# Kernel optimization log

Measured on AMD Instinct MI355X. Metric: run time of the kernel, lower is better.

The kernel has to match this reference:

```python
import jax, jax.numpy as jnp
import numpy as np

N_ATOMS, N_UND, N_DIR, N_ANG, N_STRUCT = 8192, 65536, 131072, 262144, 128
FEA, NRAD, NANGB, NCONV = 64, 9, 9, 4

FLOAT_NAMES = ["bond_bases_ag", "bond_bases_bg", "angle_bases", "atom_emb", "Wb", "Wa",
               "Wbw_ag", "Wbw_bg",
               "ac_cw1", "ac_cb1", "ac_cw2", "ac_cb2", "ac_gw1", "ac_gb1", "ac_gw2", "ac_gb2", "ac_out",
               "bc_cw1", "bc_cb1", "bc_cw2", "bc_cb2", "bc_gw1", "bc_gb1", "bc_gw2", "bc_gb2", "bc_out",
               "an_cw", "an_cb", "an_gw", "an_gb",
               "ro_w1", "ro_b1", "ro_w2", "ro_b2", "ro_w3", "ro_b3"]
INT_NAMES = ["atomic_numbers", "atom_graph", "directed2undirected",
             "bond_graph_atoms", "bond_graph_bonds", "atom_owners"]


def _silu(x):
    return x * jax.nn.sigmoid(x)


def _gmlp(x, cw1, cb1, cw2, cb2, gw1, gb1, gw2, gb2):
    # GatedMLP (norm=None): silu(MLP_core(x)) * sigmoid(MLP_gate(x)), each MLP = Lin-silu-Lin
    core = _silu(_silu(x @ cw1 + cb1) @ cw2 + cb2)
    gate = jax.nn.sigmoid(_silu(x @ gw1 + gb1) @ gw2 + gb2)
    return core * gate


def _forward(F, I):
    seg = jax.ops.segment_sum
    atom = F["atom_emb"][I["atomic_numbers"]]            # [N, 64]
    bond = F["bond_bases_ag"] @ F["Wb"]                  # [U, 64]
    angle = F["angle_bases"] @ F["Wa"]                   # [A, 64]
    bw_ag = F["bond_bases_ag"] @ F["Wbw_ag"]             # [U, 64]
    bw_bg = F["bond_bases_bg"] @ F["Wbw_bg"]             # [U, 64]
    ag0, ag1 = I["atom_graph"][:, 0], I["atom_graph"][:, 1]
    d2u = I["directed2undirected"]
    bgi, bgj = I["bond_graph_bonds"][:, 0], I["bond_graph_bonds"][:, 1]
    bga = I["bond_graph_atoms"]

    def atom_conv(i, atom, bond):
        msg = jnp.concatenate([atom[ag0], bond[d2u], atom[ag1]], axis=1)   # [E, 192]
        msg = _gmlp(msg, F["ac_cw1"][i], F["ac_cb1"][i], F["ac_cw2"][i], F["ac_cb2"][i],
                    F["ac_gw1"][i], F["ac_gb1"][i], F["ac_gw2"][i], F["ac_gb2"][i])
        msg = msg * bw_ag[d2u]
        # scatter-add to center atoms, linear mlp_out (no bias), resnet
        return atom + seg(msg, ag0, num_segments=N_ATOMS) @ F["ac_out"][i]

    for i in range(NCONV - 1):
        atom = atom_conv(i, atom, bond)
        # BondConv over bond graph (angles)
        tot = jnp.concatenate([bond[bgi], bond[bgj], angle, atom[bga]], axis=1)  # [A, 256]
        upd = _gmlp(tot, F["bc_cw1"][i], F["bc_cb1"][i], F["bc_cw2"][i], F["bc_cb2"][i],
                    F["bc_gw1"][i], F["bc_gb1"][i], F["bc_gw2"][i], F["bc_gb2"][i])
        upd = upd * bw_bg[bgi]
        bond = bond + seg(upd, bgi, num_segments=N_UND) @ F["bc_out"][i]
        # AngleUpdate (hidden_dim=0 -> single linear in each gated branch), resnet
        tot2 = jnp.concatenate([bond[bgi], bond[bgj], angle, atom[bga]], axis=1)
        angle = angle + _silu(tot2 @ F["an_cw"][i] + F["an_cb"][i]) * \
            jax.nn.sigmoid(tot2 @ F["an_gw"][i] + F["an_gb"][i])
    atom = atom_conv(NCONV - 1, atom, bond)

    # mlp_first readout: per-atom energy MLP then average pooling per structure
    e = _silu(atom @ F["ro_w1"] + F["ro_b1"])
    e = _silu(e @ F["ro_w2"] + F["ro_b2"])
    e = (e @ F["ro_w3"] + F["ro_b3"])[:, 0]              # [N]
    owners = I["atom_owners"]
    esum = seg(e, owners, num_segments=N_STRUCT)
    cnt = seg(jnp.ones_like(e), owners, num_segments=N_STRUCT)
    return esum / jnp.maximum(cnt, 1.0)                  # [N_STRUCT] energy/atom


def setup_inputs() -> dict:
    key = jax.random.key(0)
    ks = iter(jax.random.split(key, 64))

    def nrm(shape, fan_in):
        return jax.random.normal(next(ks), shape, dtype=jnp.float32) / np.float32(np.sqrt(fan_in))

    z = lambda *s: jnp.zeros(s, dtype=jnp.float32)
    inp = {}
    inp["atomic_numbers"] = jax.random.randint(next(ks), (N_ATOMS,), 0, 94, dtype=jnp.int32)
    inp["bond_bases_ag"] = jax.random.uniform(next(ks), (N_UND, NRAD), dtype=jnp.float32)
    inp["bond_bases_bg"] = jax.random.uniform(next(ks), (N_UND, NRAD), dtype=jnp.float32)
    inp["angle_bases"] = jax.random.uniform(next(ks), (N_ANG, NANGB), dtype=jnp.float32)
    inp["atom_graph"] = jax.random.randint(next(ks), (N_DIR, 2), 0, N_ATOMS, dtype=jnp.int32)
    inp["directed2undirected"] = jax.random.randint(next(ks), (N_DIR,), 0, N_UND, dtype=jnp.int32)
    inp["bond_graph_atoms"] = jax.random.randint(next(ks), (N_ANG,), 0, N_ATOMS, dtype=jnp.int32)
    inp["bond_graph_bonds"] = jax.random.randint(next(ks), (N_ANG, 2), 0, N_UND, dtype=jnp.int32)
    inp["atom_owners"] = jnp.sort(jax.random.randint(next(ks), (N_ATOMS,), 0, N_STRUCT, dtype=jnp.int32))
    inp["atom_emb"] = nrm((95, FEA), 1.0)
    inp["Wb"] = nrm((NRAD, FEA), NRAD)
    inp["Wa"] = nrm((NANGB, FEA), NANGB)
    inp["Wbw_ag"] = nrm((NRAD, FEA), NRAD)
    inp["Wbw_bg"] = nrm((NRAD, FEA), NRAD)
    d_a, d_b = 3 * FEA, 4 * FEA
    nb = NCONV - 1
    inp["ac_cw1"] = nrm((NCONV, d_a, FEA), d_a); inp["ac_cb1"] = z(NCONV, FEA)
    inp["ac_cw2"] = nrm((NCONV, FEA, FEA), FEA); inp["ac_cb2"] = z(NCONV, FEA)
    inp["ac_gw1"] = nrm((NCONV, d_a, FEA), d_a); inp["ac_gb1"] = z(NCONV, FEA)
    inp["ac_gw2"] = nrm((NCONV, FEA, FEA), FEA); inp["ac_gb2"] = z(NCONV, FEA)
    inp["ac_out"] = nrm((NCONV, FEA, FEA), FEA)
    inp["bc_cw1"] = nrm((nb, d_b, FEA), d_b); inp["bc_cb1"] = z(nb, FEA)
    inp["bc_cw2"] = nrm((nb, FEA, FEA), FEA); inp["bc_cb2"] = z(nb, FEA)
    inp["bc_gw1"] = nrm((nb, d_b, FEA), d_b); inp["bc_gb1"] = z(nb, FEA)
    inp["bc_gw2"] = nrm((nb, FEA, FEA), FEA); inp["bc_gb2"] = z(nb, FEA)
    inp["bc_out"] = nrm((nb, FEA, FEA), FEA)
    inp["an_cw"] = nrm((nb, d_b, FEA), d_b); inp["an_cb"] = z(nb, FEA)
    inp["an_gw"] = nrm((nb, d_b, FEA), d_b); inp["an_gb"] = z(nb, FEA)
    inp["ro_w1"] = nrm((FEA, FEA), FEA); inp["ro_b1"] = z(FEA)
    inp["ro_w2"] = nrm((FEA, FEA), FEA); inp["ro_b2"] = z(FEA)
    inp["ro_w3"] = nrm((FEA, 1), FEA); inp["ro_b3"] = z(1)
    return inp


def reference(atomic_numbers, bond_bases_ag, bond_bases_bg, angle_bases, atom_graph,
              directed2undirected, bond_graph_atoms, bond_graph_bonds, atom_owners,
              atom_emb, Wb, Wa, Wbw_ag, Wbw_bg,
              ac_cw1, ac_cb1, ac_cw2, ac_cb2, ac_gw1, ac_gb1, ac_gw2, ac_gb2, ac_out,
              bc_cw1, bc_cb1, bc_cw2, bc_cb2, bc_gw1, bc_gb1, bc_gw2, bc_gb2, bc_out,
              an_cw, an_cb, an_gw, an_gb,
              ro_w1, ro_b1, ro_w2, ro_b2, ro_w3, ro_b3):
    loc = locals()
    F = {k: loc[k] for k in FLOAT_NAMES}
    I = {k: loc[k] for k in INT_NAMES}
    return _forward(F, I)
```

## Files before the change

kernel.cpp:

```cpp
#include <hip/hip_runtime.h>
#include <hip/hip_bf16.h>

typedef float f32x4 __attribute__((ext_vector_type(4)));
typedef short s16x8 __attribute__((ext_vector_type(8)));
typedef unsigned int u32x4 __attribute__((ext_vector_type(4)));

#define DEV static __device__ __forceinline__

DEV unsigned short f2bf(float x){
    unsigned u = __builtin_bit_cast(unsigned, x);
    u += 0x7FFFu + ((u >> 16) & 1u);
    return (unsigned short)(u >> 16);
}
DEV float bf2f(unsigned short h){
    unsigned u = ((unsigned)h) << 16;
    return __builtin_bit_cast(float, u);
}
DEV float sigm_(float x){ return __builtin_amdgcn_rcpf(1.0f + __expf(-x)); }
DEV float silu_(float x){ return x * sigm_(x); }

DEV int xcd_swz(){
    int bid = blockIdx.x, nwg = gridDim.x;
    return (bid & 7) * (nwg >> 3) + (bid >> 3);
}

__global__ __launch_bounds__(256) void k_transconv(const float* __restrict__ src,
                                                   unsigned short* __restrict__ dst,
                                                   int K, int total){
    int gid = blockIdx.x * 256 + threadIdx.x;
    if (gid >= total) return;
    int kn  = K * 64;
    int b   = gid / kn;
    int rem = gid - b * kn;
    int k   = rem >> 6, n = rem & 63;
    dst[b * kn + n * K + k] = f2bf(src[gid]);
}

__global__ __launch_bounds__(256) void k_embed(const float* __restrict__ emb,
                                               const int* __restrict__ z,
                                               unsigned short* __restrict__ out){
    int gid = blockIdx.x * 256 + threadIdx.x;
    int n = gid >> 6, f = gid & 63;
    out[gid] = f2bf(emb[z[n] * 64 + f]);
}

__global__ __launch_bounds__(256) void k_smallmm(const float* __restrict__ bases,
                                                 const float* __restrict__ W,
                                                 unsigned short* __restrict__ out){
    int gid = blockIdx.x * 256 + threadIdx.x;
    int r = gid >> 6, f = gid & 63;
    const float* b = bases + r * 9;
    float acc = 0.f;
    #pragma unroll
    for (int k = 0; k < 9; ++k) acc += b[k] * W[k * 64 + f];
    out[gid] = f2bf(acc);
}

__global__ void k_count(const int* __restrict__ dst, int stride, int n, int* __restrict__ cnt){
    int i = blockIdx.x * 256 + threadIdx.x;
    if (i < n) atomicAdd(&cnt[dst[(size_t)i * stride]], 1);
}

__global__ __launch_bounds__(256) void k_bsum(const int* __restrict__ cnt,
                                              int* __restrict__ bsum){
    int i = blockIdx.x * 256 + threadIdx.x;
    int v = cnt[i];
    #pragma unroll
    for (int off = 32; off > 0; off >>= 1) v += __shfl_down(v, off);
    __shared__ int ws[4];
    if ((threadIdx.x & 63) == 0) ws[threadIdx.x >> 6] = v;
    __syncthreads();
    if (threadIdx.x == 0) bsum[blockIdx.x] = ws[0] + ws[1] + ws[2] + ws[3];
}

__global__ __launch_bounds__(256) void k_bscan(const int* __restrict__ bsum,
                                               int* __restrict__ bbase, int nb,
                                               int* __restrict__ total_out){
    __shared__ int sh[256];
    int t = threadIdx.x;
    int v = (t < nb) ? bsum[t] : 0;
    sh[t] = v;
    __syncthreads();
    for (int d = 1; d < 256; d <<= 1){
        int u = (t >= d) ? sh[t - d] : 0;
        __syncthreads();
        sh[t] += u;
        __syncthreads();
    }
    if (t < nb) bbase[t] = sh[t] - v;
    if (t == nb - 1) *total_out = sh[t];
}

__global__ __launch_bounds__(256) void k_offs(const int* __restrict__ cnt,
                                              const int* __restrict__ bbase,
                                              int* __restrict__ offs){
    __shared__ int sh[256];
    int t = threadIdx.x;
    int i = blockIdx.x * 256 + t;
    int v = cnt[i];
    sh[t] = v;
    __syncthreads();
    for (int d = 1; d < 256; d <<= 1){
        int u = (t >= d) ? sh[t - d] : 0;
        __syncthreads();
        sh[t] += u;
        __syncthreads();
    }
    offs[i] = bbase[blockIdx.x] + sh[t] - v;
}

__global__ void k_fill(const int* __restrict__ dst, int stride, int n,
                       const int* __restrict__ offs, int* __restrict__ cur,
                       int* __restrict__ idx){
    int i = blockIdx.x * 256 + threadIdx.x;
    if (i < n){
        int d = dst[(size_t)i * stride];
        int p = offs[d] + atomicAdd(&cur[d], 1);
        idx[p] = i;
    }
}

__global__ __launch_bounds__(256) void k_reduce(const unsigned short* __restrict__ upd,
                                                const int* __restrict__ offs,
                                                unsigned short* __restrict__ act, int nRows){
    int gid = blockIdx.x * 256 + threadIdx.x;
    int row = gid >> 3;
    if (row >= nRows) return;
    int c8 = (gid & 7) * 8;
    int o = offs[row], e = offs[row + 1];
    float acc[8] = {};
    for (int j = o; j < e; ++j){
        s16x8 v = *(const s16x8*)&upd[(size_t)j * 64 + c8];
        #pragma unroll
        for (int q = 0; q < 8; ++q) acc[q] += bf2f((unsigned short)v[q]);
    }
    s16x8 a = *(s16x8*)&act[(size_t)row * 64 + c8];
    #pragma unroll
    for (int q = 0; q < 8; ++q) a[q] = (short)f2bf(bf2f((unsigned short)a[q]) + acc[q]);
    *(s16x8*)&act[(size_t)row * 64 + c8] = a;
}

#define MFMA16(a,b,c) __builtin_amdgcn_mfma_f32_16x16x32_bf16(a,b,c,0,0,0)

__global__ __launch_bounds__(256, 4) void k_atom_conv(
    const unsigned short* __restrict__ atomBf, const unsigned short* __restrict__ bondBf,
    const unsigned short* __restrict__ bwagBf,
    const int* __restrict__ agraph, const int* __restrict__ d2u,
    const int* __restrict__ idxA,
    const unsigned short* __restrict__ w1cT, const unsigned short* __restrict__ w1gT,
    const unsigned short* __restrict__ w2cT, const unsigned short* __restrict__ w2gT,
    const unsigned short* __restrict__ woT,
    const float* __restrict__ cb1, const float* __restrict__ cb2,
    const float* __restrict__ gb1, const float* __restrict__ gb2,
    unsigned short* __restrict__ upd)
{
    __shared__ unsigned short lds[14208];
    __shared__ unsigned short ldsBw[64 * 68];
    __shared__ int ldsSrc[256];
    unsigned short* ldsA  = lds;
    unsigned short* ldsHC = lds;
    unsigned short* ldsHG = lds + 4736;
    unsigned short* ldsV  = lds + 9472;
    const int tid = threadIdx.x;
    const int r0  = xcd_swz() * 64;

    {
        int q = tid >> 6, row = tid & 63;
        int e = idxA[r0 + row];
        int s;
        if (q == 0)      s = agraph[2 * e];
        else if (q == 1) s = d2u[e];
        else if (q == 2) s = agraph[2 * e + 1];
        else             s = d2u[e];
        ldsSrc[tid] = s;
    }
    __syncthreads();
    {
        const int lane8 = tid & 7;
        #pragma unroll
        for (int p = 0; p < 8; ++p){
            int cc = p * 32 + (tid >> 3);
            int q = cc >> 6, row = cc & 63;
            int s = ldsSrc[cc];
            const unsigned short* buf = (q == 1 || q == 3) ? bondBf : atomBf;
            if (q == 3) buf = bwagBf;
            u32x4 v = *(const u32x4*)(buf + (size_t)s * 64 + lane8 * 8);
            if (q < 3) *(u32x4*)&ldsA[row * 200 + q * 64 + lane8 * 8] = v;
            else       *(u32x4*)&ldsBw[row * 68 + lane8 * 8] = v;
        }
    }
    __syncthreads();

    const int lane = tid & 63;
    const int r16  = lane & 15;
    const int grp  = lane >> 4;
    const int col  = (tid >> 6) * 16 + r16;

    f32x4 aC[4] = {}, aG[4] = {};
    #pragma unroll
    for (int kt = 0; kt < 6; ++kt){
        s16x8 bc = *(const s16x8*)&w1cT[col * 192 + kt * 32 + grp * 8];
        s16x8 bg = *(const s16x8*)&w1gT[col * 192 + kt * 32 + grp * 8];
        #pragma unroll
        for (int mt = 0; mt < 4; ++mt){
            s16x8 a = *(const s16x8*)&ldsA[(mt * 16 + r16) * 200 + kt * 32 + grp * 8];
            aC[mt] = MFMA16(a, bc, aC[mt]);
            aG[mt] = MFMA16(a, bg, aG[mt]);
        }
    }
    __syncthreads();

    const float bC1 = cb1[col], bG1 = gb1[col];
    #pragma unroll
    for (int mt = 0; mt < 4; ++mt){
        #pragma unroll
        for (int j = 0; j < 4; ++j){
            int row = mt * 16 + grp * 4 + j;
            ldsHC[row * 74 + col] = f2bf(silu_(aC[mt][j] + bC1));
            ldsHG[row * 74 + col] = f2bf(silu_(aG[mt][j] + bG1));
        }
    }
    __syncthreads();

    f32x4 oC[4] = {}, oG[4] = {};
    #pragma unroll
    for (int kt = 0; kt < 2; ++kt){
        s16x8 bc = *(const s16x8*)&w2cT[col * 64 + kt * 32 + grp * 8];
        s16x8 bg = *(const s16x8*)&w2gT[col * 64 + kt * 32 + grp * 8];
        #pragma unroll
        for (int mt = 0; mt < 4; ++mt){
            s16x8 hc = *(const s16x8*)&ldsHC[(mt * 16 + r16) * 74 + kt * 32 + grp * 8];
            s16x8 hg = *(const s16x8*)&ldsHG[(mt * 16 + r16) * 74 + kt * 32 + grp * 8];
            oC[mt] = MFMA16(hc, bc, oC[mt]);
            oG[mt] = MFMA16(hg, bg, oG[mt]);
        }
    }
    const float bC2 = cb2[col], bG2 = gb2[col];
    #pragma unroll
    for (int mt = 0; mt < 4; ++mt){
        #pragma unroll
        for (int j = 0; j < 4; ++j){
            int row = mt * 16 + grp * 4 + j;
            float v = silu_(oC[mt][j] + bC2) * sigm_(oG[mt][j] + bG2);
            v *= bf2f(ldsBw[row * 68 + col]);
            ldsV[row * 74 + col] = f2bf(v);
        }
    }
    __syncthreads();

    f32x4 oD[4] = {};
    #pragma unroll
    for (int kt = 0; kt < 2; ++kt){
        s16x8 bo = *(const s16x8*)&woT[col * 64 + kt * 32 + grp * 8];
        #pragma unroll
        for (int mt = 0; mt < 4; ++mt){
            s16x8 a = *(const s16x8*)&ldsV[(mt * 16 + r16) * 74 + kt * 32 + grp * 8];
            oD[mt] = MFMA16(a, bo, oD[mt]);
        }
    }
    #pragma unroll
    for (int mt = 0; mt < 4; ++mt){
        #pragma unroll
        for (int j = 0; j < 4; ++j){
            int row = mt * 16 + grp * 4 + j;
            upd[(size_t)(r0 + row) * 64 + col] = f2bf(oD[mt][j]);
        }
    }
}

__global__ __launch_bounds__(256, 4) void k_bond_conv(
    const unsigned short* __restrict__ atomBf, const unsigned short* __restrict__ bondBf,
    const unsigned short* __restrict__ angleBf, const unsigned short* __restrict__ bwbgBf,
    const int* __restrict__ bga, const int* __restrict__ bgb,
    const int* __restrict__ idxB,
    const unsigned short* __restrict__ w1cT, const unsigned short* __restrict__ w1gT,
    const unsigned short* __restrict__ w2cT, const unsigned short* __restrict__ w2gT,
    const unsigned short* __restrict__ woT,
    const float* __restrict__ cb1, const float* __restrict__ cb2,
    const float* __restrict__ gb1, const float* __restrict__ gb2,
    unsigned short* __restrict__ upd)
{
    __shared__ unsigned short lds[16896];
    __shared__ int ldsSrc[256];
    unsigned short* ldsA  = lds;
    unsigned short* ldsHC = lds;
    unsigned short* ldsHG = lds + 4736;
    unsigned short* ldsV  = lds + 9472;
    const int tid = threadIdx.x;
    const int r0  = xcd_swz() * 64;

    {
        int q = tid >> 6, row = tid & 63;
        int a = idxB[r0 + row];
        int s;
        if (q == 0)      s = bgb[2 * a];
        else if (q == 1) s = bgb[2 * a + 1];
        else if (q == 2) s = a;
        else             s = bga[a];
        ldsSrc[tid] = s;
    }
    __syncthreads();
    {
        const int lane8 = tid & 7;
        #pragma unroll
        for (int p = 0; p < 8; ++p){
            int cc = p * 32 + (tid >> 3);
            int q = cc >> 6, row = cc & 63;
            int s = ldsSrc[cc];
            const unsigned short* buf = (q < 2) ? bondBf : (q == 2 ? angleBf : atomBf);
            u32x4 v = *(const u32x4*)(buf + (size_t)s * 64 + lane8 * 8);
            *(u32x4*)&ldsA[row * 264 + q * 64 + lane8 * 8] = v;
        }
    }
    __syncthreads();

    const int lane = tid & 63;
    const int r16  = lane & 15;
    const int grp  = lane >> 4;
    const int col  = (tid >> 6) * 16 + r16;

    unsigned short bwv[16];
    #pragma unroll
    for (int mt = 0; mt < 4; ++mt)
        #pragma unroll
        for (int j = 0; j < 4; ++j)
            bwv[mt * 4 + j] = bwbgBf[(size_t)ldsSrc[mt * 16 + grp * 4 + j] * 64 + col];

    f32x4 aC[4] = {}, aG[4] = {};
    #pragma unroll
    for (int kt = 0; kt < 8; ++kt){
        s16x8 bc = *(const s16x8*)&w1cT[col * 256 + kt * 32 + grp * 8];
        s16x8 bg = *(const s16x8*)&w1gT[col * 256 + kt * 32 + grp * 8];
        #pragma unroll
        for (int mt = 0; mt < 4; ++mt){
            s16x8 a = *(const s16x8*)&ldsA[(mt * 16 + r16) * 264 + kt * 32 + grp * 8];
            aC[mt] = MFMA16(a, bc, aC[mt]);
            aG[mt] = MFMA16(a, bg, aG[mt]);
        }
    }
    __syncthreads();

    const float bC1 = cb1[col], bG1 = gb1[col];
    #pragma unroll
    for (int mt = 0; mt < 4; ++mt){
        #pragma unroll
        for (int j = 0; j < 4; ++j){
            int row = mt * 16 + grp * 4 + j;
            ldsHC[row * 74 + col] = f2bf(silu_(aC[mt][j] + bC1));
            ldsHG[row * 74 + col] = f2bf(silu_(aG[mt][j] + bG1));
        }
    }
    __syncthreads();

    f32x4 oC[4] = {}, oG[4] = {};
    #pragma unroll
    for (int kt = 0; kt < 2; ++kt){
        s16x8 bc = *(const s16x8*)&w2cT[col * 64 + kt * 32 + grp * 8];
        s16x8 bg = *(const s16x8*)&w2gT[col * 64 + kt * 32 + grp * 8];
        #pragma unroll
        for (int mt = 0; mt < 4; ++mt){
            s16x8 hc = *(const s16x8*)&ldsHC[(mt * 16 + r16) * 74 + kt * 32 + grp * 8];
            s16x8 hg = *(const s16x8*)&ldsHG[(mt * 16 + r16) * 74 + kt * 32 + grp * 8];
            oC[mt] = MFMA16(hc, bc, oC[mt]);
            oG[mt] = MFMA16(hg, bg, oG[mt]);
        }
    }
    const float bC2 = cb2[col], bG2 = gb2[col];
    #pragma unroll
    for (int mt = 0; mt < 4; ++mt){
        #pragma unroll
        for (int j = 0; j < 4; ++j){
            int row = mt * 16 + grp * 4 + j;
            float v = silu_(oC[mt][j] + bC2) * sigm_(oG[mt][j] + bG2);
            v *= bf2f(bwv[mt * 4 + j]);
            ldsV[row * 74 + col] = f2bf(v);
        }
    }
    __syncthreads();

    f32x4 oD[4] = {};
    #pragma unroll
    for (int kt = 0; kt < 2; ++kt){
        s16x8 bo = *(const s16x8*)&woT[col * 64 + kt * 32 + grp * 8];
        #pragma unroll
        for (int mt = 0; mt < 4; ++mt){
            s16x8 a = *(const s16x8*)&ldsV[(mt * 16 + r16) * 74 + kt * 32 + grp * 8];
            oD[mt] = MFMA16(a, bo, oD[mt]);
        }
    }
    #pragma unroll
    for (int mt = 0; mt < 4; ++mt){
        #pragma unroll
        for (int j = 0; j < 4; ++j){
            int row = mt * 16 + grp * 4 + j;
            upd[(size_t)(r0 + row) * 64 + col] = f2bf(oD[mt][j]);
        }
    }
}

__global__ __launch_bounds__(256, 4) void k_angle(
    const unsigned short* __restrict__ atomBf, const unsigned short* __restrict__ bondBf,
    unsigned short* __restrict__ angleBf,
    const int* __restrict__ bga, const int* __restrict__ bgb,
    const int* __restrict__ idxB,
    const unsigned short* __restrict__ wcT, const unsigned short* __restrict__ wgT,
    const float* __restrict__ cb, const float* __restrict__ gb)
{
    __shared__ unsigned short ldsA[64 * 264];
    __shared__ int ldsSrc[256];
    const int tid = threadIdx.x;
    const int r0  = xcd_swz() * 64;

    {
        int q = tid >> 6, row = tid & 63;
        int a = idxB[r0 + row];
        int s;
        if (q == 0)      s = bgb[2 * a];
        else if (q == 1) s = bgb[2 * a + 1];
        else if (q == 2) s = a;
        else             s = bga[a];
        ldsSrc[tid] = s;
    }
    __syncthreads();
    {
        const int lane8 = tid & 7;
        #pragma unroll
        for (int p = 0; p < 8; ++p){
            int cc = p * 32 + (tid >> 3);
            int q = cc >> 6, row = cc & 63;
            int s = ldsSrc[cc];
            const unsigned short* buf = (q < 2) ? bondBf : (q == 2 ? angleBf : atomBf);
            u32x4 v = *(const u32x4*)(buf + (size_t)s * 64 + lane8 * 8);
            *(u32x4*)&ldsA[row * 264 + q * 64 + lane8 * 8] = v;
        }
    }
    __syncthreads();

    const int lane = tid & 63;
    const int r16  = lane & 15;
    const int grp  = lane >> 4;
    const int col  = (tid >> 6) * 16 + r16;

    f32x4 aC[4] = {}, aG[4] = {};
    #pragma unroll
    for (int kt = 0; kt < 8; ++kt){
        s16x8 bc = *(const s16x8*)&wcT[col * 256 + kt * 32 + grp * 8];
        s16x8 bg = *(const s16x8*)&wgT[col * 256 + kt * 32 + grp * 8];
        #pragma unroll
        for (int mt = 0; mt < 4; ++mt){
            s16x8 a = *(const s16x8*)&ldsA[(mt * 16 + r16) * 264 + kt * 32 + grp * 8];
            aC[mt] = MFMA16(a, bc, aC[mt]);
            aG[mt] = MFMA16(a, bg, aG[mt]);
        }
    }
    const float bC = cb[col], bG = gb[col];
    #pragma unroll
    for (int mt = 0; mt < 4; ++mt){
        #pragma unroll
        for (int j = 0; j < 4; ++j){
            int row = mt * 16 + grp * 4 + j;
            int a = ldsSrc[128 + row];
            float oldv = bf2f(ldsA[row * 264 + 128 + col]);
            float v = silu_(aC[mt][j] + bC) * sigm_(aG[mt][j] + bG);
            angleBf[(size_t)a * 64 + col] = f2bf(oldv + v);
        }
    }
}

__global__ __launch_bounds__(256) void k_readout(
    const unsigned short* __restrict__ atomBf, const int* __restrict__ owners,
    const float* __restrict__ w1, const float* __restrict__ b1,
    const float* __restrict__ w2, const float* __restrict__ b2,
    const float* __restrict__ w3, const float* __restrict__ b3,
    float* __restrict__ esum, float* __restrict__ cnt)
{
    int gid  = blockIdx.x * 256 + threadIdx.x;
    int n    = gid >> 6;
    int lane = threadIdx.x & 63;
    float a = bf2f(atomBf[n * 64 + lane]);
    float acc = b1[lane];
    #pragma unroll
    for (int k = 0; k < 64; ++k) acc += __shfl(a, k) * w1[k * 64 + lane];
    float h = silu_(acc);
    acc = b2[lane];
    #pragma unroll
    for (int k = 0; k < 64; ++k) acc += __shfl(h, k) * w2[k * 64 + lane];
    h = silu_(acc);
    float p = h * w3[lane];
    #pragma unroll
    for (int off = 32; off > 0; off >>= 1) p += __shfl_xor(p, off);
    if (lane == 0){
        atomicAdd(&esum[owners[n]], p + b3[0]);
        atomicAdd(&cnt[owners[n]], 1.0f);
    }
}

__global__ void k_final(const float* __restrict__ esum, const float* __restrict__ cnt,
                        float* __restrict__ out){
    int i = threadIdx.x;
    if (i < 128) out[i] = esum[i] / fmaxf(cnt[i], 1.0f);
}

extern "C" void kernel_launch(void* const* d_in, const int* in_sizes, int n_in,
                              void* d_out, int out_size, void* d_ws, size_t ws_size,
                              hipStream_t stream)
{
    (void)in_sizes; (void)n_in; (void)out_size; (void)ws_size;
    const int N_ATOMS = 8192, N_UND = 65536, N_DIR = 131072, N_ANG = 262144;

    const int*   atomic_numbers = (const int*)  d_in[0];
    const float* bb_ag  = (const float*)d_in[1];
    const float* bb_bg  = (const float*)d_in[2];
    const float* ang_b  = (const float*)d_in[3];
    const int*   agraph = (const int*)  d_in[4];
    const int*   d2u    = (const int*)  d_in[5];
    const int*   bga    = (const int*)  d_in[6];
    const int*   bgb    = (const int*)  d_in[7];
    const int*   owners = (const int*)  d_in[8];
    const float* emb    = (const float*)d_in[9];
    const float* Wb     = (const float*)d_in[10];
    const float* Wa     = (const float*)d_in[11];
    const float* Wbwag  = (const float*)d_in[12];
    const float* Wbwbg  = (const float*)d_in[13];
    const float* ac_cw1 = (const float*)d_in[14];
    const float* ac_cb1 = (const float*)d_in[15];
    const float* ac_cw2 = (const float*)d_in[16];
    const float* ac_cb2 = (const float*)d_in[17];
    const float* ac_gw1 = (const float*)d_in[18];
    const float* ac_gb1 = (const float*)d_in[19];
    const float* ac_gw2 = (const float*)d_in[20];
    const float* ac_gb2 = (const float*)d_in[21];
    const float* ac_out = (const float*)d_in[22];
    const float* bc_cw1 = (const float*)d_in[23];
    const float* bc_cb1 = (const float*)d_in[24];
    const float* bc_cw2 = (const float*)d_in[25];
    const float* bc_cb2 = (const float*)d_in[26];
    const float* bc_gw1 = (const float*)d_in[27];
    const float* bc_gb1 = (const float*)d_in[28];
    const float* bc_gw2 = (const float*)d_in[29];
    const float* bc_gb2 = (const float*)d_in[30];
    const float* bc_out = (const float*)d_in[31];
    const float* an_cw  = (const float*)d_in[32];
    const float* an_cb  = (const float*)d_in[33];
    const float* an_gw  = (const float*)d_in[34];
    const float* an_gb  = (const float*)d_in[35];
    const float* ro_w1  = (const float*)d_in[36];
    const float* ro_b1  = (const float*)d_in[37];
    const float* ro_w2  = (const float*)d_in[38];
    const float* ro_b2  = (const float*)d_in[39];
    const float* ro_w3  = (const float*)d_in[40];
    const float* ro_b3  = (const float*)d_in[41];

    char* ws = (char*)d_ws;
    size_t off = 0;
    auto alloc = [&](size_t bytes) -> void* {
        void* p = ws + off;
        off = (off + bytes + 255) & ~(size_t)255;
        return p;
    };
    unsigned short* atomBf  = (unsigned short*)alloc((size_t)N_ATOMS * 64 * 2);
    unsigned short* bondBf  = (unsigned short*)alloc((size_t)N_UND   * 64 * 2);
    unsigned short* angleBf = (unsigned short*)alloc((size_t)N_ANG   * 64 * 2);
    unsigned short* bwagBf  = (unsigned short*)alloc((size_t)N_UND   * 64 * 2);
    unsigned short* bwbgBf  = (unsigned short*)alloc((size_t)N_UND   * 64 * 2);
    unsigned short* updBuf  = (unsigned short*)alloc((size_t)N_ANG   * 64 * 2);
    float* esum   = (float*)alloc(128 * 4);
    float* cnt    = (float*)alloc(128 * 4);
    int* offsA = (int*)alloc((N_ATOMS + 1) * 4);
    int* curA  = (int*)alloc(N_ATOMS * 4);
    int* idxA  = (int*)alloc((size_t)N_DIR * 4);
    int* offsB = (int*)alloc((N_UND + 1) * 4);
    int* curB  = (int*)alloc(N_UND * 4);
    int* idxB  = (int*)alloc((size_t)N_ANG * 4);
    int* bsum  = (int*)alloc(256 * 4);
    int* bbase = (int*)alloc(256 * 4);
    unsigned short* acw1cT = (unsigned short*)alloc((size_t)4 * 64 * 192 * 2);
    unsigned short* acw1gT = (unsigned short*)alloc((size_t)4 * 64 * 192 * 2);
    unsigned short* acw2cT = (unsigned short*)alloc((size_t)4 * 64 * 64 * 2);
    unsigned short* acw2gT = (unsigned short*)alloc((size_t)4 * 64 * 64 * 2);
    unsigned short* acoT   = (unsigned short*)alloc((size_t)4 * 64 * 64 * 2);
    unsigned short* bcw1cT = (unsigned short*)alloc((size_t)3 * 64 * 256 * 2);
    unsigned short* bcw1gT = (unsigned short*)alloc((size_t)3 * 64 * 256 * 2);
    unsigned short* bcw2cT = (unsigned short*)alloc((size_t)3 * 64 * 64 * 2);
    unsigned short* bcw2gT = (unsigned short*)alloc((size_t)3 * 64 * 64 * 2);
    unsigned short* bcoT   = (unsigned short*)alloc((size_t)3 * 64 * 64 * 2);
    unsigned short* anwcT  = (unsigned short*)alloc((size_t)3 * 64 * 256 * 2);
    unsigned short* anwgT  = (unsigned short*)alloc((size_t)3 * 64 * 256 * 2);

    auto tc = [&](const float* src, unsigned short* dst, int B, int K){
        int total = B * K * 64;
        k_transconv<<<(total + 255) / 256, 256, 0, stream>>>(src, dst, K, total);
    };
    tc(ac_cw1, acw1cT, 4, 192);  tc(ac_gw1, acw1gT, 4, 192);
    tc(ac_cw2, acw2cT, 4, 64);   tc(ac_gw2, acw2gT, 4, 64);
    tc(ac_out, acoT,   4, 64);
    tc(bc_cw1, bcw1cT, 3, 256);  tc(bc_gw1, bcw1gT, 3, 256);
    tc(bc_cw2, bcw2cT, 3, 64);   tc(bc_gw2, bcw2gT, 3, 64);
    tc(bc_out, bcoT,   3, 64);
    tc(an_cw,  anwcT,  3, 256);  tc(an_gw,  anwgT,  3, 256);

    k_embed<<<N_ATOMS * 64 / 256, 256, 0, stream>>>(emb, atomic_numbers, atomBf);
    k_smallmm<<<N_UND * 64 / 256, 256, 0, stream>>>(bb_ag, Wb,    bondBf);
    k_smallmm<<<N_ANG * 64 / 256, 256, 0, stream>>>(ang_b, Wa,    angleBf);
    k_smallmm<<<N_UND * 64 / 256, 256, 0, stream>>>(bb_ag, Wbwag, bwagBf);
    k_smallmm<<<N_UND * 64 / 256, 256, 0, stream>>>(bb_bg, Wbwbg, bwbgBf);

    hipMemsetAsync(curA, 0, N_ATOMS * 4, stream);
    k_count<<<(N_DIR + 255) / 256, 256, 0, stream>>>(agraph, 2, N_DIR, curA);
    k_bsum <<<N_ATOMS / 256, 256, 0, stream>>>(curA, bsum);
    k_bscan<<<1, 256, 0, stream>>>(bsum, bbase, N_ATOMS / 256, offsA + N_ATOMS);
    k_offs <<<N_ATOMS / 256, 256, 0, stream>>>(curA, bbase, offsA);
    hipMemsetAsync(curA, 0, N_ATOMS * 4, stream);
    k_fill<<<(N_DIR + 255) / 256, 256, 0, stream>>>(agraph, 2, N_DIR, offsA, curA, idxA);

    hipMemsetAsync(curB, 0, N_UND * 4, stream);
    k_count<<<(N_ANG + 255) / 256, 256, 0, stream>>>(bgb, 2, N_ANG, curB);
    k_bsum <<<N_UND / 256, 256, 0, stream>>>(curB, bsum);
    k_bscan<<<1, 256, 0, stream>>>(bsum, bbase, N_UND / 256, offsB + N_UND);
    k_offs <<<N_UND / 256, 256, 0, stream>>>(curB, bbase, offsB);
    hipMemsetAsync(curB, 0, N_UND * 4, stream);
    k_fill<<<(N_ANG + 255) / 256, 256, 0, stream>>>(bgb, 2, N_ANG, offsB, curB, idxB);

    for (int i = 0; i < 4; ++i){
        k_atom_conv<<<N_DIR / 64, 256, 0, stream>>>(
            atomBf, bondBf, bwagBf, agraph, d2u, idxA,
            acw1cT + (size_t)i * 64 * 192, acw1gT + (size_t)i * 64 * 192,
            acw2cT + (size_t)i * 64 * 64,  acw2gT + (size_t)i * 64 * 64,
            acoT   + (size_t)i * 64 * 64,
            ac_cb1 + i * 64, ac_cb2 + i * 64, ac_gb1 + i * 64, ac_gb2 + i * 64, updBuf);
        k_reduce<<<N_ATOMS * 8 / 256, 256, 0, stream>>>(updBuf, offsA, atomBf, N_ATOMS);
        if (i == 3) break;
        k_bond_conv<<<N_ANG / 64, 256, 0, stream>>>(
            atomBf, bondBf, angleBf, bwbgBf, bga, bgb, idxB,
            bcw1cT + (size_t)i * 64 * 256, bcw1gT + (size_t)i * 64 * 256,
            bcw2cT + (size_t)i * 64 * 64,  bcw2gT + (size_t)i * 64 * 64,
            bcoT   + (size_t)i * 64 * 64,
            bc_cb1 + i * 64, bc_cb2 + i * 64, bc_gb1 + i * 64, bc_gb2 + i * 64, updBuf);
        k_reduce<<<N_UND * 8 / 256, 256, 0, stream>>>(updBuf, offsB, bondBf, N_UND);
        k_angle<<<N_ANG / 64, 256, 0, stream>>>(
            atomBf, bondBf, angleBf, bga, bgb, idxB,
            anwcT + (size_t)i * 64 * 256, anwgT + (size_t)i * 64 * 256,
            an_cb + i * 64, an_gb + i * 64);
    }

    hipMemsetAsync(esum, 0, 128 * 4, stream);
    hipMemsetAsync(cnt,  0, 128 * 4, stream);
    k_readout<<<N_ATOMS * 64 / 256, 256, 0, stream>>>(
        atomBf, owners, ro_w1, ro_b1, ro_w2, ro_b2, ro_w3, ro_b3, esum, cnt);
    k_final<<<1, 128, 0, stream>>>(esum, cnt, (float*)d_out);
}
```

Baseline: 870.9 us.

## Store angles in bond-sorted order and fuse angle update with next atom conv

Angle features are now built directly in the idxB-sorted order, so the bond conv and angle kernels read them with contiguous indices instead of gathering, and the angle update writes back without a scatter. The angle update and the following atom conv, which are independent, run as one combined launch with the block range split between the two bodies. This saves launches and fills the GPU better, at the cost of shared-memory sizing set by the larger body and the loss of XCD swizzling in the fused kernel. The fused atom path writes updBuf while angle blocks only touch angleS, so there is no conflict.

```diff
diff --git a/kernel.cpp b/kernel.cpp
--- a/kernel.cpp
+++ b/kernel.cpp
@@ -50,6 +50,19 @@
     int gid = blockIdx.x * 256 + threadIdx.x;
     int r = gid >> 6, f = gid & 63;
     const float* b = bases + r * 9;
+    float acc = 0.f;
+    #pragma unroll
+    for (int k = 0; k < 9; ++k) acc += b[k] * W[k * 64 + f];
+    out[gid] = f2bf(acc);
+}
+
+__global__ __launch_bounds__(256) void k_smallmm_perm(const float* __restrict__ bases,
+                                                      const float* __restrict__ W,
+                                                      const int* __restrict__ perm,
+                                                      unsigned short* __restrict__ out){
+    int gid = blockIdx.x * 256 + threadIdx.x;
+    int r = gid >> 6, f = gid & 63;
+    const float* b = bases + (size_t)perm[r] * 9;
     float acc = 0.f;
     #pragma unroll
     for (int k = 0; k < 9; ++k) acc += b[k] * W[k * 64 + f];
@@ -141,6 +154,195 @@
 }
 
 #define MFMA16(a,b,c) __builtin_amdgcn_mfma_f32_16x16x32_bf16(a,b,c,0,0,0)
+
+DEV void atom_body(unsigned short* smem, int* ldsSrc, int bid,
+    const unsigned short* atomBf, const unsigned short* bondBf,
+    const unsigned short* bwagBf,
+    const int* agraph, const int* d2u, const int* idxA,
+    const unsigned short* w1cT, const unsigned short* w1gT,
+    const unsigned short* w2cT, const unsigned short* w2gT,
+    const unsigned short* woT,
+    const float* cb1, const float* cb2, const float* gb1, const float* gb2,
+    unsigned short* upd)
+{
+    unsigned short* ldsA  = smem;
+    unsigned short* ldsHC = smem;
+    unsigned short* ldsHG = smem + 4736;
+    unsigned short* ldsV  = smem + 9472;
+    unsigned short* ldsBw = smem + 14208;
+    const int tid = threadIdx.x;
+    const int r0  = bid * 64;
+
+    {
+        int q = tid >> 6, row = tid & 63;
+        int e = idxA[r0 + row];
+        int s;
+        if (q == 0)      s = agraph[2 * e];
+        else if (q == 1) s = d2u[e];
+        else if (q == 2) s = agraph[2 * e + 1];
+        else             s = d2u[e];
+        ldsSrc[tid] = s;
+    }
+    __syncthreads();
+    {
+        const int lane8 = tid & 7;
+        #pragma unroll
+        for (int p = 0; p < 8; ++p){
+            int cc = p * 32 + (tid >> 3);
+            int q = cc >> 6, row = cc & 63;
+            int s = ldsSrc[cc];
+            const unsigned short* buf = (q == 1 || q == 3) ? bondBf : atomBf;
+            if (q == 3) buf = bwagBf;
+            u32x4 v = *(const u32x4*)(buf + (size_t)s * 64 + lane8 * 8);
+            if (q < 3) *(u32x4*)&ldsA[row * 200 + q * 64 + lane8 * 8] = v;
+            else       *(u32x4*)&ldsBw[row * 68 + lane8 * 8] = v;
+        }
+    }
+    __syncthreads();
+
+    const int lane = tid & 63;
+    const int r16  = lane & 15;
+    const int grp  = lane >> 4;
+    const int col  = (tid >> 6) * 16 + r16;
+
+    f32x4 aC[4] = {}, aG[4] = {};
+    #pragma unroll
+    for (int kt = 0; kt < 6; ++kt){
+        s16x8 bc = *(const s16x8*)&w1cT[col * 192 + kt * 32 + grp * 8];
+        s16x8 bg = *(const s16x8*)&w1gT[col * 192 + kt * 32 + grp * 8];
+        #pragma unroll
+        for (int mt = 0; mt < 4; ++mt){
+            s16x8 a = *(const s16x8*)&ldsA[(mt * 16 + r16) * 200 + kt * 32 + grp * 8];
+            aC[mt] = MFMA16(a, bc, aC[mt]);
+            aG[mt] = MFMA16(a, bg, aG[mt]);
+        }
+    }
+    __syncthreads();
+
+    const float bC1 = cb1[col], bG1 = gb1[col];
+    #pragma unroll
+    for (int mt = 0; mt < 4; ++mt){
+        #pragma unroll
+        for (int j = 0; j < 4; ++j){
+            int row = mt * 16 + grp * 4 + j;
+            ldsHC[row * 74 + col] = f2bf(silu_(aC[mt][j] + bC1));
+            ldsHG[row * 74 + col] = f2bf(silu_(aG[mt][j] + bG1));
+        }
+    }
+    __syncthreads();
+
+    f32x4 oC[4] = {}, oG[4] = {};
+    #pragma unroll
+    for (int kt = 0; kt < 2; ++kt){
+        s16x8 bc = *(const s16x8*)&w2cT[col * 64 + kt * 32 + grp * 8];
+        s16x8 bg = *(const s16x8*)&w2gT[col * 64 + kt * 32 + grp * 8];
+        #pragma unroll
+        for (int mt = 0; mt < 4; ++mt){
+            s16x8 hc = *(const s16x8*)&ldsHC[(mt * 16 + r16) * 74 + kt * 32 + grp * 8];
+            s16x8 hg = *(const s16x8*)&ldsHG[(mt * 16 + r16) * 74 + kt * 32 + grp * 8];
+            oC[mt] = MFMA16(hc, bc, oC[mt]);
+            oG[mt] = MFMA16(hg, bg, oG[mt]);
+        }
+    }
+    const float bC2 = cb2[col], bG2 = gb2[col];
+    #pragma unroll
+    for (int mt = 0; mt < 4; ++mt){
+        #pragma unroll
+        for (int j = 0; j < 4; ++j){
+            int row = mt * 16 + grp * 4 + j;
+            float v = silu_(oC[mt][j] + bC2) * sigm_(oG[mt][j] + bG2);
+            v *= bf2f(ldsBw[row * 68 + col]);
+            ldsV[row * 74 + col] = f2bf(v);
+        }
+    }
+    __syncthreads();
+
+    f32x4 oD[4] = {};
+    #pragma unroll
+    for (int kt = 0; kt < 2; ++kt){
+        s16x8 bo = *(const s16x8*)&woT[col * 64 + kt * 32 + grp * 8];
+        #pragma unroll
+        for (int mt = 0; mt < 4; ++mt){
+            s16x8 a = *(const s16x8*)&ldsV[(mt * 16 + r16) * 74 + kt * 32 + grp * 8];
+            oD[mt] = MFMA16(a, bo, oD[mt]);
+        }
+    }
+    #pragma unroll
+    for (int mt = 0; mt < 4; ++mt){
+        #pragma unroll
+        for (int j = 0; j < 4; ++j){
+            int row = mt * 16 + grp * 4 + j;
+            upd[(size_t)(r0 + row) * 64 + col] = f2bf(oD[mt][j]);
+        }
+    }
+}
+
+DEV void angle_body(unsigned short* ldsA, int* ldsSrc, int bid,
+    const unsigned short* atomBf, const unsigned short* bondBf,
+    unsigned short* angleS,
+    const int* bga, const int* bgb, const int* idxB,
+    const unsigned short* wcT, const unsigned short* wgT,
+    const float* cb, const float* gb)
+{
+    const int tid = threadIdx.x;
+    const int r0  = bid * 64;
+
+    {
+        int q = tid >> 6, row = tid & 63;
+        int s;
+        if (q == 2) s = r0 + row;
+        else {
+            int a = idxB[r0 + row];
+            if (q == 0)      s = bgb[2 * a];
+            else if (q == 1) s = bgb[2 * a + 1];
+            else             s = bga[a];
+        }
+        ldsSrc[tid] = s;
+    }
+    __syncthreads();
+    {
+        const int lane8 = tid & 7;
+        #pragma unroll
+        for (int p = 0; p < 8; ++p){
+            int cc = p * 32 + (tid >> 3);
+            int q = cc >> 6, row = cc & 63;
+            int s = ldsSrc[cc];
+            const unsigned short* buf = (q < 2) ? bondBf : (q == 2 ? angleS : atomBf);
+            u32x4 v = *(const u32x4*)(buf + (size_t)s * 64 + lane8 * 8);
+            *(u32x4*)&ldsA[row * 264 + q * 64 + lane8 * 8] = v;
+        }
+    }
+    __syncthreads();
+
+    const int lane = tid & 63;
+    const int r16  = lane & 15;
+    const int grp  = lane >> 4;
+    const int col  = (tid >> 6) * 16 + r16;
+
+    f32x4 aC[4] = {}, aG[4] = {};
+    #pragma unroll
+    for (int kt = 0; kt < 8; ++kt){
+        s16x8 bc = *(const s16x8*)&wcT[col * 256 + kt * 32 + grp * 8];
+        s16x8 bg = *(const s16x8*)&wgT[col * 256 + kt * 32 + grp * 8];
+        #pragma unroll
+        for (int mt = 0; mt < 4; ++mt){
+            s16x8 a = *(const s16x8*)&ldsA[(mt * 16 + r16) * 264 + kt * 32 + grp * 8];
+            aC[mt] = MFMA16(a, bc, aC[mt]);
+            aG[mt] = MFMA16(a, bg, aG[mt]);
+        }
+    }
+    const float bC = cb[col], bG = gb[col];
+    #pragma unroll
+    for (int mt = 0; mt < 4; ++mt){
+        #pragma unroll
+        for (int j = 0; j < 4; ++j){
+            int row = mt * 16 + grp * 4 + j;
+            float oldv = bf2f(ldsA[row * 264 + 128 + col]);
+            float v = silu_(aC[mt][j] + bC) * sigm_(aG[mt][j] + bG);
+            angleS[(size_t)(r0 + row) * 64 + col] = f2bf(oldv + v);
+        }
+    }
+}
 
 __global__ __launch_bounds__(256, 4) void k_atom_conv(
     const unsigned short* __restrict__ atomBf, const unsigned short* __restrict__ bondBf,
@@ -154,123 +356,44 @@
     const float* __restrict__ gb1, const float* __restrict__ gb2,
     unsigned short* __restrict__ upd)
 {
-    __shared__ unsigned short lds[14208];
-    __shared__ unsigned short ldsBw[64 * 68];
+    __shared__ __align__(16) unsigned short smem[18560];
     __shared__ int ldsSrc[256];
-    unsigned short* ldsA  = lds;
-    unsigned short* ldsHC = lds;
-    unsigned short* ldsHG = lds + 4736;
-    unsigned short* ldsV  = lds + 9472;
-    const int tid = threadIdx.x;
-    const int r0  = xcd_swz() * 64;
-
-    {
-        int q = tid >> 6, row = tid & 63;
-        int e = idxA[r0 + row];
-        int s;
-        if (q == 0)      s = agraph[2 * e];
-        else if (q == 1) s = d2u[e];
-        else if (q == 2) s = agraph[2 * e + 1];
-        else             s = d2u[e];
-        ldsSrc[tid] = s;
-    }
-    __syncthreads();
-    {
-        const int lane8 = tid & 7;
-        #pragma unroll
-        for (int p = 0; p < 8; ++p){
-            int cc = p * 32 + (tid >> 3);
-            int q = cc >> 6, row = cc & 63;
-            int s = ldsSrc[cc];
-            const unsigned short* buf = (q == 1 || q == 3) ? bondBf : atomBf;
-            if (q == 3) buf = bwagBf;
-            u32x4 v = *(const u32x4*)(buf + (size_t)s * 64 + lane8 * 8);
-            if (q < 3) *(u32x4*)&ldsA[row * 200 + q * 64 + lane8 * 8] = v;
-            else       *(u32x4*)&ldsBw[row * 68 + lane8 * 8] = v;
-        }
-    }
-    __syncthreads();
-
-    const int lane = tid & 63;
-    const int r16  = lane & 15;
-    const int grp  = lane >> 4;
-    const int col  = (tid >> 6) * 16 + r16;
-
-    f32x4 aC[4] = {}, aG[4] = {};
-    #pragma unroll
-    for (int kt = 0; kt < 6; ++kt){
-        s16x8 bc = *(const s16x8*)&w1cT[col * 192 + kt * 32 + grp * 8];
-        s16x8 bg = *(const s16x8*)&w1gT[col * 192 + kt * 32 + grp * 8];
-        #pragma unroll
-        for (int mt = 0; mt < 4; ++mt){
-            s16x8 a = *(const s16x8*)&ldsA[(mt * 16 + r16) * 200 + kt * 32 + grp * 8];
-            aC[mt] = MFMA16(a, bc, aC[mt]);
-            aG[mt] = MFMA16(a, bg, aG[mt]);
-        }
-    }
-    __syncthreads();
-
-    const float bC1 = cb1[col], bG1 = gb1[col];
-    #pragma unroll
-    for (int mt = 0; mt < 4; ++mt){
-        #pragma unroll
-        for (int j = 0; j < 4; ++j){
-            int row = mt * 16 + grp * 4 + j;
-            ldsHC[row * 74 + col] = f2bf(silu_(aC[mt][j] + bC1));
-            ldsHG[row * 74 + col] = f2bf(silu_(aG[mt][j] + bG1));
-        }
-    }
-    __syncthreads();
-
-    f32x4 oC[4] = {}, oG[4] = {};
-    #pragma unroll
-    for (int kt = 0; kt < 2; ++kt){
-        s16x8 bc = *(const s16x8*)&w2cT[col * 64 + kt * 32 + grp * 8];
-        s16x8 bg = *(const s16x8*)&w2gT[col * 64 + kt * 32 + grp * 8];
-        #pragma unroll
-        for (int mt = 0; mt < 4; ++mt){
-            s16x8 hc = *(const s16x8*)&ldsHC[(mt * 16 + r16) * 74 + kt * 32 + grp * 8];
-            s16x8 hg = *(const s16x8*)&ldsHG[(mt * 16 + r16) * 74 + kt * 32 + grp * 8];
-            oC[mt] = MFMA16(hc, bc, oC[mt]);
-            oG[mt] = MFMA16(hg, bg, oG[mt]);
-        }
-    }
-    const float bC2 = cb2[col], bG2 = gb2[col];
-    #pragma unroll
-    for (int mt = 0; mt < 4; ++mt){
-        #pragma unroll
-        for (int j = 0; j < 4; ++j){
-            int row = mt * 16 + grp * 4 + j;
-            float v = silu_(oC[mt][j] + bC2) * sigm_(oG[mt][j] + bG2);
-            v *= bf2f(ldsBw[row * 68 + col]);
-            ldsV[row * 74 + col] = f2bf(v);
-        }
-    }
-    __syncthreads();
-
-    f32x4 oD[4] = {};
-    #pragma unroll
-    for (int kt = 0; kt < 2; ++kt){
-        s16x8 bo = *(const s16x8*)&woT[col * 64 + kt * 32 + grp * 8];
-        #pragma unroll
-        for (int mt = 0; mt < 4; ++mt){
-            s16x8 a = *(const s16x8*)&ldsV[(mt * 16 + r16) * 74 + kt * 32 + grp * 8];
-            oD[mt] = MFMA16(a, bo, oD[mt]);
-        }
-    }
-    #pragma unroll
-    for (int mt = 0; mt < 4; ++mt){
-        #pragma unroll
-        for (int j = 0; j < 4; ++j){
-            int row = mt * 16 + grp * 4 + j;
-            upd[(size_t)(r0 + row) * 64 + col] = f2bf(oD[mt][j]);
-        }
+    atom_body(smem, ldsSrc, xcd_swz(),
+              atomBf, bondBf, bwagBf, agraph, d2u, idxA,
+              w1cT, w1gT, w2cT, w2gT, woT, cb1, cb2, gb1, gb2, upd);
+}
+
+__global__ __launch_bounds__(256, 4) void k_angle_atom(
+    const unsigned short* __restrict__ atomBf, const unsigned short* __restrict__ bondBf,
+    unsigned short* __restrict__ angleS, const unsigned short* __restrict__ bwagBf,
+    const int* __restrict__ agraph, const int* __restrict__ d2u, const int* __restrict__ idxA,
+    const int* __restrict__ bga, const int* __restrict__ bgb, const int* __restrict__ idxB,
+    const unsigned short* __restrict__ an_wcT, const unsigned short* __restrict__ an_wgT,
+    const float* __restrict__ an_cb, const float* __restrict__ an_gb,
+    const unsigned short* __restrict__ ac_w1cT, const unsigned short* __restrict__ ac_w1gT,
+    const unsigned short* __restrict__ ac_w2cT, const unsigned short* __restrict__ ac_w2gT,
+    const unsigned short* __restrict__ ac_woT,
+    const float* __restrict__ ac_cb1, const float* __restrict__ ac_cb2,
+    const float* __restrict__ ac_gb1, const float* __restrict__ ac_gb2,
+    unsigned short* __restrict__ upd, int nbAngle)
+{
+    __shared__ __align__(16) unsigned short smem[18560];
+    __shared__ int ldsSrc[256];
+    int bid = blockIdx.x;
+    if (bid < nbAngle){
+        angle_body(smem, ldsSrc, bid, atomBf, bondBf, angleS, bga, bgb, idxB,
+                   an_wcT, an_wgT, an_cb, an_gb);
+    } else {
+        atom_body(smem, ldsSrc, bid - nbAngle,
+                  atomBf, bondBf, bwagBf, agraph, d2u, idxA,
+                  ac_w1cT, ac_w1gT, ac_w2cT, ac_w2gT, ac_woT,
+                  ac_cb1, ac_cb2, ac_gb1, ac_gb2, upd);
     }
 }
 
 __global__ __launch_bounds__(256, 4) void k_bond_conv(
     const unsigned short* __restrict__ atomBf, const unsigned short* __restrict__ bondBf,
-    const unsigned short* __restrict__ angleBf, const unsigned short* __restrict__ bwbgBf,
+    const unsigned short* __restrict__ angleS, const unsigned short* __restrict__ bwbgBf,
     const int* __restrict__ bga, const int* __restrict__ bgb,
     const int* __restrict__ idxB,
     const unsigned short* __restrict__ w1cT, const unsigned short* __restrict__ w1gT,
@@ -280,7 +403,7 @@
     const float* __restrict__ gb1, const float* __restrict__ gb2,
     unsigned short* __restrict__ upd)
 {
-    __shared__ unsigned short lds[16896];
+    __shared__ __align__(16) unsigned short lds[16896];
     __shared__ int ldsSrc[256];
     unsigned short* ldsA  = lds;
     unsigned short* ldsHC = lds;
@@ -291,12 +414,14 @@
 
     {
         int q = tid >> 6, row = tid & 63;
-        int a = idxB[r0 + row];
         int s;
-        if (q == 0)      s = bgb[2 * a];
-        else if (q == 1) s = bgb[2 * a + 1];
-        else if (q == 2) s = a;
-        else             s = bga[a];
+        if (q == 2) s = r0 + row;
+        else {
+            int a = idxB[r0 + row];
+            if (q == 0)      s = bgb[2 * a];
+            else if (q == 1) s = bgb[2 * a + 1];
+            else             s = bga[a];
+        }
         ldsSrc[tid] = s;
     }
     __syncthreads();
@@ -307,7 +432,7 @@
             int cc = p * 32 + (tid >> 3);
             int q = cc >> 6, row = cc & 63;
             int s = ldsSrc[cc];
-            const unsigned short* buf = (q < 2) ? bondBf : (q == 2 ? angleBf : atomBf);
+            const unsigned short* buf = (q < 2) ? bondBf : (q == 2 ? angleS : atomBf);
             u32x4 v = *(const u32x4*)(buf + (size_t)s * 64 + lane8 * 8);
             *(u32x4*)&ldsA[row * 264 + q * 64 + lane8 * 8] = v;
         }
@@ -394,75 +519,6 @@
         for (int j = 0; j < 4; ++j){
             int row = mt * 16 + grp * 4 + j;
             upd[(size_t)(r0 + row) * 64 + col] = f2bf(oD[mt][j]);
-        }
-    }
-}
-
-__global__ __launch_bounds__(256, 4) void k_angle(
-    const unsigned short* __restrict__ atomBf, const unsigned short* __restrict__ bondBf,
-    unsigned short* __restrict__ angleBf,
-    const int* __restrict__ bga, const int* __restrict__ bgb,
-    const int* __restrict__ idxB,
-    const unsigned short* __restrict__ wcT, const unsigned short* __restrict__ wgT,
-    const float* __restrict__ cb, const float* __restrict__ gb)
-{
-    __shared__ unsigned short ldsA[64 * 264];
-    __shared__ int ldsSrc[256];
-    const int tid = threadIdx.x;
-    const int r0  = xcd_swz() * 64;
-
-    {
-        int q = tid >> 6, row = tid & 63;
-        int a = idxB[r0 + row];
-        int s;
-        if (q == 0)      s = bgb[2 * a];
-        else if (q == 1) s = bgb[2 * a + 1];
-        else if (q == 2) s = a;
-        else             s = bga[a];
-        ldsSrc[tid] = s;
-    }
-    __syncthreads();
-    {
-        const int lane8 = tid & 7;
-        #pragma unroll
-        for (int p = 0; p < 8; ++p){
-            int cc = p * 32 + (tid >> 3);
-            int q = cc >> 6, row = cc & 63;
-            int s = ldsSrc[cc];
-            const unsigned short* buf = (q < 2) ? bondBf : (q == 2 ? angleBf : atomBf);
-            u32x4 v = *(const u32x4*)(buf + (size_t)s * 64 + lane8 * 8);
-            *(u32x4*)&ldsA[row * 264 + q * 64 + lane8 * 8] = v;
-        }
-    }
-    __syncthreads();
-
-    const int lane = tid & 63;
-    const int r16  = lane & 15;
-    const int grp  = lane >> 4;
-    const int col  = (tid >> 6) * 16 + r16;
-
-    f32x4 aC[4] = {}, aG[4] = {};
-    #pragma unroll
-    for (int kt = 0; kt < 8; ++kt){
-        s16x8 bc = *(const s16x8*)&wcT[col * 256 + kt * 32 + grp * 8];
-        s16x8 bg = *(const s16x8*)&wgT[col * 256 + kt * 32 + grp * 8];
-        #pragma unroll
-        for (int mt = 0; mt < 4; ++mt){
-            s16x8 a = *(const s16x8*)&ldsA[(mt * 16 + r16) * 264 + kt * 32 + grp * 8];
-            aC[mt] = MFMA16(a, bc, aC[mt]);
-            aG[mt] = MFMA16(a, bg, aG[mt]);
-        }
-    }
-    const float bC = cb[col], bG = gb[col];
-    #pragma unroll
-    for (int mt = 0; mt < 4; ++mt){
-        #pragma unroll
-        for (int j = 0; j < 4; ++j){
-            int row = mt * 16 + grp * 4 + j;
-            int a = ldsSrc[128 + row];
-            float oldv = bf2f(ldsA[row * 264 + 128 + col]);
-            float v = silu_(aC[mt][j] + bC) * sigm_(aG[mt][j] + bG);
-            angleBf[(size_t)a * 64 + col] = f2bf(oldv + v);
         }
     }
 }
@@ -560,7 +616,7 @@
     };
     unsigned short* atomBf  = (unsigned short*)alloc((size_t)N_ATOMS * 64 * 2);
     unsigned short* bondBf  = (unsigned short*)alloc((size_t)N_UND   * 64 * 2);
-    unsigned short* angleBf = (unsigned short*)alloc((size_t)N_ANG   * 64 * 2);
+    unsigned short* angleS  = (unsigned short*)alloc((size_t)N_ANG   * 64 * 2);
     unsigned short* bwagBf  = (unsigned short*)alloc((size_t)N_UND   * 64 * 2);
     unsigned short* bwbgBf  = (unsigned short*)alloc((size_t)N_UND   * 64 * 2);
     unsigned short* updBuf  = (unsigned short*)alloc((size_t)N_ANG   * 64 * 2);
@@ -587,6 +643,22 @@
     unsigned short* anwcT  = (unsigned short*)alloc((size_t)3 * 64 * 256 * 2);
     unsigned short* anwgT  = (unsigned short*)alloc((size_t)3 * 64 * 256 * 2);
 
+    hipMemsetAsync(curA, 0, N_ATOMS * 4, stream);
+    k_count<<<(N_DIR + 255) / 256, 256, 0, stream>>>(agraph, 2, N_DIR, curA);
+    k_bsum <<<N_ATOMS / 256, 256, 0, stream>>>(curA, bsum);
+    k_bscan<<<1, 256, 0, stream>>>(bsum, bbase, N_ATOMS / 256, offsA + N_ATOMS);
+    k_offs <<<N_ATOMS / 256, 256, 0, stream>>>(curA, bbase, offsA);
+    hipMemsetAsync(curA, 0, N_ATOMS * 4, stream);
+    k_fill<<<(N_DIR + 255) / 256, 256, 0, stream>>>(agraph, 2, N_DIR, offsA, curA, idxA);
+
+    hipMemsetAsync(curB, 0, N_UND * 4, stream);
+    k_count<<<(N_ANG + 255) / 256, 256, 0, stream>>>(bgb, 2, N_ANG, curB);
+    k_bsum <<<N_UND / 256, 256, 0, stream>>>(curB, bsum);
+    k_bscan<<<1, 256, 0, stream>>>(bsum, bbase, N_UND / 256, offsB + N_UND);
+    k_offs <<<N_UND / 256, 256, 0, stream>>>(curB, bbase, offsB);
+    hipMemsetAsync(curB, 0, N_UND * 4, stream);
+    k_fill<<<(N_ANG + 255) / 256, 256, 0, stream>>>(bgb, 2, N_ANG, offsB, curB, idxB);
+
     auto tc = [&](const float* src, unsigned short* dst, int B, int K){
         int total = B * K * 64;
         k_transconv<<<(total + 255) / 256, 256, 0, stream>>>(src, dst, K, total);
@@ -601,46 +673,38 @@
 
     k_embed<<<N_ATOMS * 64 / 256, 256, 0, stream>>>(emb, atomic_numbers, atomBf);
     k_smallmm<<<N_UND * 64 / 256, 256, 0, stream>>>(bb_ag, Wb,    bondBf);
-    k_smallmm<<<N_ANG * 64 / 256, 256, 0, stream>>>(ang_b, Wa,    angleBf);
+    k_smallmm_perm<<<N_ANG * 64 / 256, 256, 0, stream>>>(ang_b, Wa, idxB, angleS);
     k_smallmm<<<N_UND * 64 / 256, 256, 0, stream>>>(bb_ag, Wbwag, bwagBf);
     k_smallmm<<<N_UND * 64 / 256, 256, 0, stream>>>(bb_bg, Wbwbg, bwbgBf);
 
-    hipMemsetAsync(curA, 0, N_ATOMS * 4, stream);
-    k_count<<<(N_DIR + 255) / 256, 256, 0, stream>>>(agraph, 2, N_DIR, curA);
-    k_bsum <<<N_ATOMS / 256, 256, 0, stream>>>(curA, bsum);
-    k_bscan<<<1, 256, 0, stream>>>(bsum, bbase, N_ATOMS / 256, offsA + N_ATOMS);
-    k_offs <<<N_ATOMS / 256, 256, 0, stream>>>(curA, bbase, offsA);
-    hipMemsetAsync(curA, 0, N_ATOMS * 4, stream);
-    k_fill<<<(N_DIR + 255) / 256, 256, 0, stream>>>(agraph, 2, N_DIR, offsA, curA, idxA);
-
-    hipMemsetAsync(curB, 0, N_UND * 4, stream);
-    k_count<<<(N_ANG + 255) / 256, 256, 0, stream>>>(bgb, 2, N_ANG, curB);
-    k_bsum <<<N_UND / 256, 256, 0, stream>>>(curB, bsum);
-    k_bscan<<<1, 256, 0, stream>>>(bsum, bbase, N_UND / 256, offsB + N_UND);
-    k_offs <<<N_UND / 256, 256, 0, stream>>>(curB, bbase, offsB);
-    hipMemsetAsync(curB, 0, N_UND * 4, stream);
-    k_fill<<<(N_ANG + 255) / 256, 256, 0, stream>>>(bgb, 2, N_ANG, offsB, curB, idxB);
-
-    for (int i = 0; i < 4; ++i){
-        k_atom_conv<<<N_DIR / 64, 256, 0, stream>>>(
-            atomBf, bondBf, bwagBf, agraph, d2u, idxA,
-            acw1cT + (size_t)i * 64 * 192, acw1gT + (size_t)i * 64 * 192,
-            acw2cT + (size_t)i * 64 * 64,  acw2gT + (size_t)i * 64 * 64,
-            acoT   + (size_t)i * 64 * 64,
-            ac_cb1 + i * 64, ac_cb2 + i * 64, ac_gb1 + i * 64, ac_gb2 + i * 64, updBuf);
-        k_reduce<<<N_ATOMS * 8 / 256, 256, 0, stream>>>(updBuf, offsA, atomBf, N_ATOMS);
-        if (i == 3) break;
-        k_bond_conv<<<N_ANG / 64, 256, 0, stream>>>(
-            atomBf, bondBf, angleBf, bwbgBf, bga, bgb, idxB,
+    k_atom_conv<<<N_DIR / 64, 256, 0, stream>>>(
+        atomBf, bondBf, bwagBf, agraph, d2u, idxA,
+        acw1cT, acw1gT, acw2cT, acw2gT, acoT,
+        ac_cb1, ac_cb2, ac_gb1, ac_gb2, updBuf);
+    k_reduce<<<N_ATOMS * 8 / 256, 256, 0, stream>>>(updBuf, offsA, atomBf, N_ATOMS);
+
+    const int NB_AN = N_ANG / 64;
+    const int NB_AC = N_DIR / 64;
+    for (int i = 0; i < 3; ++i){
+        k_bond_conv<<<NB_AN, 256, 0, stream>>>(
+            atomBf, bondBf, angleS, bwbgBf, bga, bgb, idxB,
             bcw1cT + (size_t)i * 64 * 256, bcw1gT + (size_t)i * 64 * 256,
             bcw2cT + (size_t)i * 64 * 64,  bcw2gT + (size_t)i * 64 * 64,
             bcoT   + (size_t)i * 64 * 64,
             bc_cb1 + i * 64, bc_cb2 + i * 64, bc_gb1 + i * 64, bc_gb2 + i * 64, updBuf);
         k_reduce<<<N_UND * 8 / 256, 256, 0, stream>>>(updBuf, offsB, bondBf, N_UND);
-        k_angle<<<N_ANG / 64, 256, 0, stream>>>(
-            atomBf, bondBf, angleBf, bga, bgb, idxB,
+        k_angle_atom<<<NB_AN + NB_AC, 256, 0, stream>>>(
+            atomBf, bondBf, angleS, bwagBf,
+            agraph, d2u, idxA, bga, bgb, idxB,
             anwcT + (size_t)i * 64 * 256, anwgT + (size_t)i * 64 * 256,
-            an_cb + i * 64, an_gb + i * 64);
+            an_cb + i * 64, an_gb + i * 64,
+            acw1cT + (size_t)(i + 1) * 64 * 192, acw1gT + (size_t)(i + 1) * 64 * 192,
+            acw2cT + (size_t)(i + 1) * 64 * 64,  acw2gT + (size_t)(i + 1) * 64 * 64,
+            acoT   + (size_t)(i + 1) * 64 * 64,
+            ac_cb1 + (i + 1) * 64, ac_cb2 + (i + 1) * 64,
+            ac_gb1 + (i + 1) * 64, ac_gb2 + (i + 1) * 64,
+            updBuf, NB_AN);
+        k_reduce<<<N_ATOMS * 8 / 256, 256, 0, stream>>>(updBuf, offsA, atomBf, N_ATOMS);
     }
 
     hipMemsetAsync(esum, 0, 128 * 4, stream);
```

After: 859.4 us. About the same (-1.3%).
